# Kernel optimization log

Measured on AMD Instinct MI355X. Metric: run time of the kernel, lower is better.

## Reference

```python
import jax, jax.numpy as jnp
import numpy as np

B, T, D, H, WIN = 4, 2048, 512, 8, 128
DK = D // H
DFF = 4 * D
LN_EPS = 1e-5


def setup_inputs() -> dict:
    key = jax.random.key(0)
    ks = jax.random.split(key, 12)
    p = lambda k, shp: jax.random.normal(k, shp, jnp.float32) * 0.02
    return {
        "x": jax.random.normal(ks[0], (B, T, D), jnp.float32),
        "pad_mask": jnp.ones((B, T), dtype=bool),
        "wq": p(ks[1], (D, D)), "bq": jnp.zeros((D,), jnp.float32),
        "wk": p(ks[2], (D, D)), "bk": jnp.zeros((D,), jnp.float32),
        "wv": p(ks[3], (D, D)), "bv": jnp.zeros((D,), jnp.float32),
        "wo": p(ks[4], (D, D)), "bo": jnp.zeros((D,), jnp.float32),
        "w1": p(ks[5], (D, DFF)), "b1": jnp.zeros((DFF,), jnp.float32),
        "w2": p(ks[6], (DFF, D)), "b2": jnp.zeros((D,), jnp.float32),
        "g1": jnp.ones((D,), jnp.float32), "be1": jnp.zeros((D,), jnp.float32),
        "g2": jnp.ones((D,), jnp.float32), "be2": jnp.zeros((D,), jnp.float32),
    }


def _ln(x, g, b):
    m = x.mean(-1, keepdims=True)
    v = ((x - m) ** 2).mean(-1, keepdims=True)
    return (x - m) * jax.lax.rsqrt(v + LN_EPS) * g + b


def reference(x, pad_mask, wq, bq, wk, bk, wv, bv, wo, bo,
              w1, b1, w2, b2, g1, be1, g2, be2):
    Bv, Tv, Dv = x.shape
    # projections -> [B, H, T, DK]
    q = (x @ wq + bq).reshape(Bv, Tv, H, DK).transpose(0, 2, 1, 3)
    k = (x @ wk + bk).reshape(Bv, Tv, H, DK).transpose(0, 2, 1, 3)
    v = (x @ wv + bv).reshape(Bv, Tv, H, DK).transpose(0, 2, 1, 3)
    idx = jnp.arange(Tv)
    dist = idx[None, :] - idx[:, None]  # q rows, k cols? matches torch: idx[None,:]-idx[:,None] with rows=q
    wmask = (dist >= 0) & (dist < WIN)  # note: dist = k - q in torch code orientation; see original
    # original: dist = idx[None,:] - idx[:,None]; window_mask[q, k] = (k - q >= 0)&(k - q < W)? No:
    # torch uses dist[q, k] = idx[None,:][q,k] - idx[:,None][q,k] = k - q, mask (dist>=0)&(dist<W)
    # so key index >= query index within window — reproduce exactly.
    mask = pad_mask[:, None, None, :] & wmask[None, None, :, :]  # [B,1,T,T]
    scores = jnp.einsum('bhqd,bhkd->bhqk', q, k) / np.float32(np.sqrt(DK))
    scores = jnp.where(mask, scores, jnp.float32(-1e9))
    attn = jax.nn.softmax(scores, axis=-1)
    o = jnp.einsum('bhqk,bhkd->bhqd', attn, v)
    o = o.transpose(0, 2, 1, 3).reshape(Bv, Tv, Dv)
    attn_out = o @ wo + bo
    x1 = _ln(x + attn_out, g1, be1)
    ff = jax.nn.relu(x1 @ w1 + b1) @ w2 + b2
    return _ln(x1 + ff, g2, be2)
```

## Files before the change

### kernel.cpp

```cpp
#include <hip/hip_runtime.h>

typedef __bf16 bf16;
typedef float  f32x4  __attribute__((ext_vector_type(4)));
typedef __bf16 bf16x8 __attribute__((ext_vector_type(8)));
typedef __bf16 bf16x4 __attribute__((ext_vector_type(4)));

#define GLOAD_LDS16(gsrc, ldst) \
  __builtin_amdgcn_global_load_lds((const __attribute__((address_space(1))) void*)(gsrc), \
                                   (__attribute__((address_space(3))) void*)(ldst), 16, 0, 0)

constexpr int Bc   = 4;
constexpr int Tc   = 2048;
constexpr int Dc   = 512;
constexpr int Hc   = 8;
constexpr int DKc  = 64;
constexpr int DFFc = 2048;
constexpr int WINc = 128;
constexpr int Mr   = Bc * Tc;
constexpr size_t MD = (size_t)Mr * Dc;
constexpr int TVc  = 2176;

__device__ bf16  g_xb[MD];
__device__ bf16  g_wqkvT[3 * Dc * Dc];
__device__ bf16  g_woT[Dc * Dc];
__device__ bf16  g_w1T[DFFc * Dc];
__device__ bf16  g_w2T[Dc * DFFc];
__device__ float g_biasqkv[3 * Dc];
__device__ bf16  g_qkv[Mr * 3 * Dc];
__device__ bf16  g_vT[(size_t)Bc * Hc * DKc * TVc];
__device__ bf16  g_o[MD];
__device__ bf16  g_attnp[2 * MD];
__device__ bf16  g_x1b[MD];
__device__ bf16  g_ff1[Mr * DFFc];
__device__ bf16  g_ff2p[4 * MD];

__global__ __launch_bounds__(256) void prep_k(const float* __restrict__ x,
                                              const float* __restrict__ wq, const float* __restrict__ wk,
                                              const float* __restrict__ wv, const float* __restrict__ wo,
                                              const float* __restrict__ w1, const float* __restrict__ w2,
                                              const float* __restrict__ bq, const float* __restrict__ bk,
                                              const float* __restrict__ bv) {
  int bid = blockIdx.x;
  if (bid < 2048) {
    size_t i = (size_t)bid * 2048 + threadIdx.x * 8;
    float4 a = *(const float4*)(x + i);
    float4 c = *(const float4*)(x + i + 4);
    bf16x8 o;
    o[0] = (bf16)a.x; o[1] = (bf16)a.y; o[2] = (bf16)a.z; o[3] = (bf16)a.w;
    o[4] = (bf16)c.x; o[5] = (bf16)c.y; o[6] = (bf16)c.z; o[7] = (bf16)c.w;
    *(bf16x8*)(g_xb + i) = o;
    return;
  }
  if (bid >= 5120) {
    int i = (bid - 5120) * 256 + threadIdx.x;
    if (i < 1536) g_biasqkv[i] = (i < 512) ? bq[i] : (i < 1024 ? bk[i - 512] : bv[i - 1024]);
    return;
  }
  const float* W; bf16* dst; int K, N, nx, ky;
  if (bid < 3072) {
    int local = bid - 2048;
    int wsel = local >> 8; local &= 255;
    nx = local & 15; ky = local >> 4; K = 512; N = 512;
    switch (wsel) {
      case 0: W = wq; dst = g_wqkvT;              break;
      case 1: W = wk; dst = g_wqkvT + 512 * 512;  break;
      case 2: W = wv; dst = g_wqkvT + 1024 * 512; break;
      default:W = wo; dst = g_woT;                break;
    }
  } else if (bid < 4096) {
    int local = bid - 3072;
    nx = local & 63; ky = local >> 6; K = 512; N = 2048; W = w1; dst = g_w1T;
  } else {
    int local = bid - 4096;
    nx = local & 15; ky = local >> 4; K = 2048; N = 512; W = w2; dst = g_w2T;
  }
  __shared__ float t[32][33];
  int n0 = nx * 32, k0 = ky * 32;
  int tx = threadIdx.x & 31, ty = threadIdx.x >> 5;
  #pragma unroll
  for (int i = 0; i < 4; ++i)
    t[ty + i * 8][tx] = W[(size_t)(k0 + ty + i * 8) * N + n0 + tx];
  __syncthreads();
  #pragma unroll
  for (int i = 0; i < 4; ++i)
    dst[(size_t)(n0 + ty + i * 8) * K + k0 + tx] = (bf16)t[tx][ty + i * 8];
}

__global__ __launch_bounds__(512, 2) void gemm8p_k(int which, const float* __restrict__ bias_in) {
  const bf16 *A, *BT; bf16* Cb; const float* bias;
  int N, K; bool relu = false;
  int kz = blockIdx.z;
  if (which == 0)      { A = g_xb;  BT = g_wqkvT; Cb = g_qkv; bias = g_biasqkv; N = 1536; K = 512; }
  else if (which == 2) { A = g_x1b; BT = g_w1T;   Cb = g_ff1; bias = bias_in;   N = 2048; K = 512; relu = true; }
  else                 { A = g_ff1; BT = g_w2T;   Cb = g_ff2p + (size_t)kz * MD; bias = bias_in; N = 512; K = 2048; }
  if (kz) bias = nullptr;
  const int kzoff = kz * 512;
  constexpr int NT = 8;

  __shared__ __align__(16) bf16 lds[65536];

  const int tid = threadIdx.x;
  const int bm = blockIdx.x, bn = blockIdx.y;
  const int w = tid >> 6, lane = tid & 63;
  const int wm = w >> 2, wn = w & 3;
  const int r = lane & 15, gg = lane >> 4;

  const bf16* gA0 = A  + (size_t)(bm * 256) * K + kzoff;
  const bf16* gB0 = BT + (size_t)(bn * 256) * K + kzoff;

  f32x4 acc[8][4] = {};

  auto stageHalf = [&](int S) {
    if (S >= 4 * NT) return;
    const int tau = S >> 2, h = S & 3, buf = tau & 1;
    const int colT = tau * 64;
    if (h >= 2) {
      const int ks = h - 2;
      char* dst = (char*)lds + buf * 65536 + ks * 16384 + w * 1024;
      #pragma unroll
      for (int swp = 0; swp < 2; ++swp) {
        int s = swp * 512 + tid;
        int row = s >> 2;
        int cb = (s & 3) ^ (((row >> 1) ^ (row >> 3)) & 3);
        GLOAD_LDS16(gA0 + (size_t)row * K + colT + ks * 32 + cb * 8, dst + swp * 8192);
      }
    } else {
      char* dst = (char*)lds + buf * 65536 + 32768 + h * 16384 + w * 1024;
      #pragma unroll
      for (int swp = 0; swp < 2; ++swp) {
        int s = swp * 512 + tid;
        int row = h * 128 + (s >> 3);
        int cb = (s & 7) ^ (row & 7);
        GLOAD_LDS16(gB0 + (size_t)row * K + colT + cb * 8, dst + swp * 8192);
      }
    }
  };

  #pragma unroll
  for (int S = 0; S < 7; ++S) stageHalf(S);
  asm volatile("s_waitcnt vmcnt(6)" ::: "memory");
  __builtin_amdgcn_s_barrier();

  #pragma unroll
  for (int t = 0; t < NT; ++t) {
    const bf16* lb = lds + (t & 1) * 32768;
    bf16x8 b0[4], b1[4], afr[4];

    #pragma unroll
    for (int ni = 0; ni < 4; ++ni) {
      int row = wn * 64 + ni * 16 + r;
      b0[ni] = *(const bf16x8*)(lb + 16384 + row * 64 + ((gg ^ (r & 7)) << 3));
      b1[ni] = *(const bf16x8*)(lb + 16384 + row * 64 + (((4 + gg) ^ (r & 7)) << 3));
    }
    #pragma unroll
    for (int i = 0; i < 4; ++i) {
      int row = wm * 128 + i * 16 + r;
      afr[i] = *(const bf16x8*)(lb + row * 32 + ((gg ^ (((row >> 1) ^ (row >> 3)) & 3)) << 3));
    }
    asm volatile("" ::: "memory");
    stageHalf(4 * t + 7);
    __builtin_amdgcn_s_barrier();
    __builtin_amdgcn_s_setprio(1);
    #pragma unroll
    for (int i = 0; i < 4; ++i)
      #pragma unroll
      for (int ni = 0; ni < 4; ++ni)
        acc[i][ni] = __builtin_amdgcn_mfma_f32_16x16x32_bf16(afr[i], b0[ni], acc[i][ni], 0, 0, 0);
    __builtin_amdgcn_s_setprio(0);
    __builtin_amdgcn_s_barrier();

    #pragma unroll
    for (int i = 0; i < 4; ++i) {
      int row = wm * 128 + 64 + i * 16 + r;
      afr[i] = *(const bf16x8*)(lb + row * 32 + ((gg ^ (((row >> 1) ^ (row >> 3)) & 3)) << 3));
    }
    asm volatile("" ::: "memory");
    stageHalf(4 * t + 8);
    __builtin_amdgcn_s_barrier();
    __builtin_amdgcn_s_setprio(1);
    #pragma unroll
    for (int i = 0; i < 4; ++i)
      #pragma unroll
      for (int ni = 0; ni < 4; ++ni)
        acc[4 + i][ni] = __builtin_amdgcn_mfma_f32_16x16x32_bf16(afr[i], b0[ni], acc[4 + i][ni], 0, 0, 0);
    __builtin_amdgcn_s_setprio(0);
    __builtin_amdgcn_s_barrier();

    #pragma unroll
    for (int i = 0; i < 4; ++i) {
      int row = wm * 128 + i * 16 + r;
      afr[i] = *(const bf16x8*)(lb + 8192 + row * 32 + ((gg ^ (((row >> 1) ^ (row >> 3)) & 3)) << 3));
    }
    asm volatile("" ::: "memory");
    stageHalf(4 * t + 9);
    __builtin_amdgcn_s_barrier();
    __builtin_amdgcn_s_setprio(1);
    #pragma unroll
    for (int i = 0; i < 4; ++i)
      #pragma unroll
      for (int ni = 0; ni < 4; ++ni)
        acc[i][ni] = __builtin_amdgcn_mfma_f32_16x16x32_bf16(afr[i], b1[ni], acc[i][ni], 0, 0, 0);
    __builtin_amdgcn_s_setprio(0);
    __builtin_amdgcn_s_barrier();

    #pragma unroll
    for (int i = 0; i < 4; ++i) {
      int row = wm * 128 + 64 + i * 16 + r;
      afr[i] = *(const bf16x8*)(lb + 8192 + row * 32 + ((gg ^ (((row >> 1) ^ (row >> 3)) & 3)) << 3));
    }
    asm volatile("" ::: "memory");
    stageHalf(4 * t + 10);
    if (t < NT - 2)       asm volatile("s_waitcnt vmcnt(6)" ::: "memory");
    else if (t == NT - 2) asm volatile("s_waitcnt vmcnt(0)" ::: "memory");
    __builtin_amdgcn_s_barrier();
    __builtin_amdgcn_s_setprio(1);
    #pragma unroll
    for (int i = 0; i < 4; ++i)
      #pragma unroll
      for (int ni = 0; ni < 4; ++ni)
        acc[4 + i][ni] = __builtin_amdgcn_mfma_f32_16x16x32_bf16(afr[i], b1[ni], acc[4 + i][ni], 0, 0, 0);
    __builtin_amdgcn_s_setprio(0);
    __builtin_amdgcn_s_barrier();
  }

  if (which == 0 && bn >= 4) {
    #pragma unroll
    for (int mi = 0; mi < 8; ++mi) {
      int row0 = bm * 256 + wm * 128 + mi * 16 + gg * 4;
      int bidx = row0 >> 11, t0 = row0 & 2047;
      #pragma unroll
      for (int ni = 0; ni < 4; ++ni) {
        int col = bn * 256 + wn * 64 + ni * 16 + r;
        float bv = bias[col];
        int vcol = col - 1024;
        bf16x4 ov;
        #pragma unroll
        for (int j = 0; j < 4; ++j) ov[j] = (bf16)(acc[mi][ni][j] + bv);
        *(bf16x4*)(g_vT + (size_t)(bidx * 512 + vcol) * TVc + t0) = ov;
      }
    }
    return;
  }
  #pragma unroll
  for (int mi = 0; mi < 8; ++mi) {
    int row0 = bm * 256 + wm * 128 + mi * 16 + gg * 4;
    #pragma unroll
    for (int ni = 0; ni < 4; ++ni) {
      int col = bn * 256 + wn * 64 + ni * 16 + r;
      float bv = bias ? bias[col] : 0.f;
      #pragma unroll
      for (int j = 0; j < 4; ++j) {
        float v0 = acc[mi][ni][j] + bv;
        if (relu) v0 = fmaxf(v0, 0.f);
        Cb[(size_t)(row0 + j) * N + col] = (bf16)v0;
      }
    }
  }
}

__global__ __launch_bounds__(256) void gemm_k(const float* __restrict__ bias_in) {
  const bf16 *A, *BT;
  bf16* Cb;
  const float* bias;
  int N, K, Klen;
  int kz = blockIdx.z;
  { A = g_o; BT = g_woT; Cb = g_attnp + (size_t)kz * MD; bias = bias_in; N = 512; K = 512; Klen = 256; }
  if (kz) bias = nullptr;

  __shared__ __align__(16) bf16 lA[128 * 32];
  __shared__ __align__(16) bf16 lB[128 * 32];
  int tid = threadIdx.x;
  int bm = blockIdx.x, bn = blockIdx.y;
  int w = tid >> 6, lane = tid & 63;
  int wm = w >> 1, wn = w & 1;
  int r = lane & 15, gg = lane >> 4;

  f32x4 acc[4][4] = {};

  const bf16* gA = A + (size_t)(bm * 128 + (tid >> 2)) * K + (size_t)kz * Klen + (tid & 3) * 8;
  const bf16* gB = BT + (size_t)(bn * 128 + (tid >> 2)) * K + (size_t)kz * Klen + (tid & 3) * 8;
  char* lAb = (char*)lA + (tid & 0xC0) * 16;
  char* lBb = (char*)lB + (tid & 0xC0) * 16;

  for (int k0 = 0; k0 < Klen; k0 += 32) {
    GLOAD_LDS16(gA + k0,                  lAb);
    GLOAD_LDS16(gA + (size_t)64 * K + k0, lAb + 4096);
    GLOAD_LDS16(gB + k0,                  lBb);
    GLOAD_LDS16(gB + (size_t)64 * K + k0, lBb + 4096);
    asm volatile("s_waitcnt vmcnt(0)" ::: "memory");
    __syncthreads();
    bf16x8 afrag[4], bfrag[4];
    #pragma unroll
    for (int i = 0; i < 4; ++i)
      afrag[i] = *(const bf16x8*)(&lA[(wm * 64 + i * 16 + r) * 32 + gg * 8]);
    #pragma unroll
    for (int i = 0; i < 4; ++i)
      bfrag[i] = *(const bf16x8*)(&lB[(wn * 64 + i * 16 + r) * 32 + gg * 8]);
    #pragma unroll
    for (int mi = 0; mi < 4; ++mi)
      #pragma unroll
      for (int ni = 0; ni < 4; ++ni)
        acc[mi][ni] = __builtin_amdgcn_mfma_f32_16x16x32_bf16(afrag[mi], bfrag[ni], acc[mi][ni], 0, 0, 0);
    __syncthreads();
  }

  #pragma unroll
  for (int mi = 0; mi < 4; ++mi) {
    int row0 = bm * 128 + wm * 64 + mi * 16 + gg * 4;
    #pragma unroll
    for (int ni = 0; ni < 4; ++ni) {
      int col = bn * 128 + wn * 64 + ni * 16 + r;
      float bv = bias ? bias[col] : 0.f;
      #pragma unroll
      for (int j = 0; j < 4; ++j) {
        float v0 = acc[mi][ni][j] + bv;
        Cb[(size_t)(row0 + j) * N + col] = (bf16)v0;
      }
    }
  }
}

__global__ __launch_bounds__(256) void attn_k() {
  constexpr int KT = 192;
  __shared__ __align__(16) bf16 lKP[KT * 64];
  __shared__ __align__(16) bf16 lVT[64 * KT];
  int tid = threadIdx.x;
  int qt = blockIdx.x, bh = blockIdx.y;
  int b = bh >> 3, h = bh & 7;
  int q0 = qt * 64;
  int w = tid >> 6, lane = tid & 63;
  int r = lane & 15, gg = lane >> 4;

  {
    const bf16* kbase = g_qkv + (size_t)b * Tc * 1536 + 512 + h * 64;
    char* ldst = (char*)lKP + w * 1024;
    #pragma unroll
    for (int p = 0; p < 6; ++p) {
      int s = p * 256 + tid;
      int key = s >> 3;
      int cb = (s & 7) ^ (key & 7);
      int gkey = q0 + key;
      int srow = gkey < Tc ? gkey : 0;
      GLOAD_LDS16(kbase + (size_t)srow * 1536 + cb * 8, ldst + p * 4096);
    }
  }
  {
    const bf16* vbase = g_vT + (size_t)(bh * 64) * TVc + q0;
    char* ldst = (char*)lVT + w * 1024;
    #pragma unroll
    for (int p = 0; p < 6; ++p) {
      int s = p * 256 + tid;
      int d = s / 24;
      int sc = s - d * 24;
      int cb = sc ^ (d & 7);
      GLOAD_LDS16(vbase + (size_t)d * TVc + cb * 8, ldst + p * 4096);
    }
  }
  bf16x8 qf0, qf1;
  {
    int qrow = q0 + w * 16 + r;
    const bf16* qp = g_qkv + (size_t)(b * Tc + qrow) * 1536 + h * 64;
    qf0 = *(const bf16x8*)(qp + gg * 8);
    qf1 = *(const bf16x8*)(qp + 32 + gg * 8);
  }
  asm volatile("s_waitcnt vmcnt(0)" ::: "memory");
  __syncthreads();

  f32x4 s[12] = {};
  #pragma unroll
  for (int ni = 0; ni < 12; ++ni) {
    int key = ni * 16 + r;
    int sw = key & 7;
    bf16x8 k0f = *(const bf16x8*)(&lKP[key * 64 + ((gg ^ sw) << 3)]);
    bf16x8 k1f = *(const bf16x8*)(&lKP[key * 64 + (((4 | gg) ^ sw) << 3)]);
    s[ni] = __builtin_amdgcn_mfma_f32_16x16x32_bf16(qf0, k0f, s[ni], 0, 0, 0);
    s[ni] = __builtin_amdgcn_mfma_f32_16x16x32_bf16(qf1, k1f, s[ni], 0, 0, 0);
  }

  float mx[4] = {-3e38f, -3e38f, -3e38f, -3e38f};
  #pragma unroll
  for (int ni = 0; ni < 12; ++ni)
    #pragma unroll
    for (int j = 0; j < 4; ++j) {
      int qloc = w * 16 + gg * 4 + j;
      int col = ni * 16 + r;
      bool valid = (col >= qloc) && (col < qloc + WINc) && (q0 + col < Tc);
      float sv = valid ? s[ni][j] * 0.125f : -3e38f;
      s[ni][j] = sv;
      mx[j] = fmaxf(mx[j], sv);
    }
  #pragma unroll
  for (int m = 1; m < 16; m <<= 1)
    #pragma unroll
    for (int j = 0; j < 4; ++j) mx[j] = fmaxf(mx[j], __shfl_xor(mx[j], m, 64));

  float sm[4] = {0.f, 0.f, 0.f, 0.f};
  #pragma unroll
  for (int ni = 0; ni < 12; ++ni)
    #pragma unroll
    for (int j = 0; j < 4; ++j) {
      float p = __expf(s[ni][j] - mx[j]);
      s[ni][j] = p;
      sm[j] += p;
    }
  #pragma unroll
  for (int m = 1; m < 16; m <<= 1)
    #pragma unroll
    for (int j = 0; j < 4; ++j) sm[j] += __shfl_xor(sm[j], m, 64);

  __syncthreads();
  #pragma unroll
  for (int ni = 0; ni < 12; ++ni)
    #pragma unroll
    for (int j = 0; j < 4; ++j) {
      int q = w * 16 + gg * 4 + j;
      int col = ni * 16 + r;
      int idx = q * KT + ((((col >> 3) ^ (q & 7)) << 3) | (col & 7));
      lKP[idx] = (bf16)s[ni][j];
    }
  __syncthreads();

  f32x4 o[4] = {};
  int swl = r & 7;
  #pragma unroll
  for (int ks = 0; ks < 6; ++ks) {
    int ch = ((ks * 4 + gg) ^ swl) << 3;
    bf16x8 pf = *(const bf16x8*)(&lKP[(w * 16 + r) * KT + ch]);
    #pragma unroll
    for (int nf = 0; nf < 4; ++nf) {
      bf16x8 vf = *(const bf16x8*)(&lVT[(nf * 16 + r) * KT + ch]);
      o[nf] = __builtin_amdgcn_mfma_f32_16x16x32_bf16(pf, vf, o[nf], 0, 0, 0);
    }
  }
  #pragma unroll
  for (int nf = 0; nf < 4; ++nf) {
    int dk = nf * 16 + r;
    #pragma unroll
    for (int j = 0; j < 4; ++j) {
      int qloc = w * 16 + gg * 4 + j;
      float ov = o[nf][j] / sm[j];
      g_o[(size_t)(b * Tc + q0 + qloc) * Dc + h * 64 + dk] = (bf16)ov;
    }
  }
}

__global__ __launch_bounds__(256) void ln_k(int which, const float* __restrict__ gw,
                                            const float* __restrict__ bw,
                                            float* __restrict__ outf_in) {
  int row = blockIdx.x * 4 + (threadIdx.x >> 6);
  int lane = threadIdx.x & 63;
  const bf16* a; const bf16* pb; int np; float* outf; bf16* outb;
  if (which == 0) { a = g_xb;  pb = g_attnp; np = 2; outf = nullptr;  outb = g_x1b; }
  else            { a = g_x1b; pb = g_ff2p;  np = 4; outf = outf_in;  outb = nullptr; }
  size_t off = (size_t)row * 512 + lane * 8;
  bf16x8 av = *(const bf16x8*)(a + off);
  float v[8];
  #pragma unroll
  for (int i = 0; i < 8; ++i) v[i] = (float)av[i];
  for (int p = 0; p < np; ++p) {
    bf16x8 t = *(const bf16x8*)(pb + (size_t)p * MD + off);
    #pragma unroll
    for (int i = 0; i < 8; ++i) v[i] += (float)t[i];
  }
  float s = 0.f;
  #pragma unroll
  for (int i = 0; i < 8; ++i) s += v[i];
  #pragma unroll
  for (int m = 1; m < 64; m <<= 1) s += __shfl_xor(s, m, 64);
  float mean = s * (1.0f / 512.0f);
  float q = 0.f;
  #pragma unroll
  for (int i = 0; i < 8; ++i) { float d = v[i] - mean; q += d * d; }
  #pragma unroll
  for (int m = 1; m < 64; m <<= 1) q += __shfl_xor(q, m, 64);
  float rstd = rsqrtf(q * (1.0f / 512.0f) + 1e-5f);
  float4 g0 = *(const float4*)(gw + lane * 8), g1v = *(const float4*)(gw + lane * 8 + 4);
  float4 e0 = *(const float4*)(bw + lane * 8), e1 = *(const float4*)(bw + lane * 8 + 4);
  float gg[8] = {g0.x, g0.y, g0.z, g0.w, g1v.x, g1v.y, g1v.z, g1v.w};
  float bb[8] = {e0.x, e0.y, e0.z, e0.w, e1.x, e1.y, e1.z, e1.w};
  float o[8];
  #pragma unroll
  for (int i = 0; i < 8; ++i) o[i] = (v[i] - mean) * rstd * gg[i] + bb[i];
  if (outf) {
    float4 o0 = {o[0], o[1], o[2], o[3]}, o1 = {o[4], o[5], o[6], o[7]};
    *(float4*)(outf + off) = o0;
    *(float4*)(outf + off + 4) = o1;
  }
  if (outb) {
    bf16x8 ob;
    #pragma unroll
    for (int i = 0; i < 8; ++i) ob[i] = (bf16)o[i];
    *(bf16x8*)(outb + off) = ob;
  }
}

extern "C" void kernel_launch(void* const* d_in, const int* in_sizes, int n_in,
                              void* d_out, int out_size, void* d_ws, size_t ws_size,
                              hipStream_t stream) {
  const float* x   = (const float*)d_in[0];
  const float* wq  = (const float*)d_in[2];
  const float* bq  = (const float*)d_in[3];
  const float* wk  = (const float*)d_in[4];
  const float* bk  = (const float*)d_in[5];
  const float* wv  = (const float*)d_in[6];
  const float* bv  = (const float*)d_in[7];
  const float* wo  = (const float*)d_in[8];
  const float* bo  = (const float*)d_in[9];
  const float* w1  = (const float*)d_in[10];
  const float* b1  = (const float*)d_in[11];
  const float* w2  = (const float*)d_in[12];
  const float* b2  = (const float*)d_in[13];
  const float* g1  = (const float*)d_in[14];
  const float* be1 = (const float*)d_in[15];
  const float* g2  = (const float*)d_in[16];
  const float* be2 = (const float*)d_in[17];
  float* out = (float*)d_out;

  prep_k<<<5126, 256, 0, stream>>>(x, wq, wk, wv, wo, w1, w2, bq, bk, bv);

  gemm8p_k<<<dim3(32, 6, 1), 512, 0, stream>>>(0, nullptr);
  attn_k<<<dim3(32, 32), 256, 0, stream>>>();
  gemm_k<<<dim3(64, 4, 2), 256, 0, stream>>>(bo);
  ln_k<<<2048, 256, 0, stream>>>(0, g1, be1, nullptr);
  gemm8p_k<<<dim3(32, 8, 1), 512, 0, stream>>>(2, b1);
  gemm8p_k<<<dim3(32, 2, 4), 512, 0, stream>>>(3, b2);
  ln_k<<<2048, 256, 0, stream>>>(1, g2, be2, out);
}
```

Measured before the change: 145.1 us.

## Remap block indices for XCD-aware L2 locality and overlap V loads in attention

Remaps the linear block id in the three GEMM/attention kernels so that consecutive blocks, which the hardware spreads round-robin across the XCDs, share A/B tiles or neighbouring query tiles on the same XCD's L2. In attention, the Q fragment loads are moved ahead of the V-tile loads, and the first barrier waits only for K (vmcnt(6)), so the QK^T and softmax work overlaps with the V transfer. The remapping assumes specific grid dimensions (32 or 64 in x), and the partial waitcnt depends on the exact count and order of outstanding loads.

```diff
diff --git a/kernel.cpp b/kernel.cpp
--- a/kernel.cpp
+++ b/kernel.cpp
@@ -87,20 +87,25 @@
 }
 
 __global__ __launch_bounds__(512, 2) void gemm8p_k(int which, const float* __restrict__ bias_in) {
+  const int h = blockIdx.x + 32 * (blockIdx.y + gridDim.y * blockIdx.z);
+  const int xc = h & 7, hi = h >> 3;
+  const int bm = xc + 8 * (hi & 3);
+  const int yz = hi >> 2;
+  const int bn = yz % gridDim.y;
+  const int kz = yz / gridDim.y;
+
   const bf16 *A, *BT; bf16* Cb; const float* bias;
   int N, K; bool relu = false;
-  int kz = blockIdx.z;
   if (which == 0)      { A = g_xb;  BT = g_wqkvT; Cb = g_qkv; bias = g_biasqkv; N = 1536; K = 512; }
   else if (which == 2) { A = g_x1b; BT = g_w1T;   Cb = g_ff1; bias = bias_in;   N = 2048; K = 512; relu = true; }
   else                 { A = g_ff1; BT = g_w2T;   Cb = g_ff2p + (size_t)kz * MD; bias = bias_in; N = 512; K = 2048; }
-  if (kz) bias = nullptr;
+  const float* bias0 = (kz == 0) ? bias : nullptr;
   const int kzoff = kz * 512;
   constexpr int NT = 8;
 
   __shared__ __align__(16) bf16 lds[65536];
 
   const int tid = threadIdx.x;
-  const int bm = blockIdx.x, bn = blockIdx.y;
   const int w = tid >> 6, lane = tid & 63;
   const int wm = w >> 2, wn = w & 3;
   const int r = lane & 15, gg = lane >> 4;
@@ -112,10 +117,10 @@
 
   auto stageHalf = [&](int S) {
     if (S >= 4 * NT) return;
-    const int tau = S >> 2, h = S & 3, buf = tau & 1;
+    const int tau = S >> 2, hh = S & 3, buf = tau & 1;
     const int colT = tau * 64;
-    if (h >= 2) {
-      const int ks = h - 2;
+    if (hh >= 2) {
+      const int ks = hh - 2;
       char* dst = (char*)lds + buf * 65536 + ks * 16384 + w * 1024;
       #pragma unroll
       for (int swp = 0; swp < 2; ++swp) {
@@ -125,11 +130,11 @@
         GLOAD_LDS16(gA0 + (size_t)row * K + colT + ks * 32 + cb * 8, dst + swp * 8192);
       }
     } else {
-      char* dst = (char*)lds + buf * 65536 + 32768 + h * 16384 + w * 1024;
+      char* dst = (char*)lds + buf * 65536 + 32768 + hh * 16384 + w * 1024;
       #pragma unroll
       for (int swp = 0; swp < 2; ++swp) {
         int s = swp * 512 + tid;
-        int row = h * 128 + (s >> 3);
+        int row = hh * 128 + (s >> 3);
         int cb = (s & 7) ^ (row & 7);
         GLOAD_LDS16(gB0 + (size_t)row * K + colT + cb * 8, dst + swp * 8192);
       }
@@ -247,7 +252,7 @@
     #pragma unroll
     for (int ni = 0; ni < 4; ++ni) {
       int col = bn * 256 + wn * 64 + ni * 16 + r;
-      float bv = bias ? bias[col] : 0.f;
+      float bv = bias0 ? bias0[col] : 0.f;
       #pragma unroll
       for (int j = 0; j < 4; ++j) {
         float v0 = acc[mi][ni][j] + bv;
@@ -259,18 +264,20 @@
 }
 
 __global__ __launch_bounds__(256) void gemm_k(const float* __restrict__ bias_in) {
-  const bf16 *A, *BT;
-  bf16* Cb;
-  const float* bias;
-  int N, K, Klen;
-  int kz = blockIdx.z;
-  { A = g_o; BT = g_woT; Cb = g_attnp + (size_t)kz * MD; bias = bias_in; N = 512; K = 512; Klen = 256; }
-  if (kz) bias = nullptr;
+  const int h = blockIdx.x + 64 * (blockIdx.y + 4 * blockIdx.z);
+  const int xc = h & 7, hi = h >> 3;
+  const int bm = xc + 8 * (hi & 7);
+  const int yz = hi >> 3;
+  const int bn = yz & 3, kz = yz >> 2;
+
+  const bf16* A = g_o; const bf16* BT = g_woT;
+  bf16* Cb = g_attnp + (size_t)kz * MD;
+  const float* bias = kz ? nullptr : bias_in;
+  const int N = 512, K = 512, Klen = 256;
 
   __shared__ __align__(16) bf16 lA[128 * 32];
   __shared__ __align__(16) bf16 lB[128 * 32];
   int tid = threadIdx.x;
-  int bm = blockIdx.x, bn = blockIdx.y;
   int w = tid >> 6, lane = tid & 63;
   int wm = w >> 1, wn = w & 1;
   int r = lane & 15, gg = lane >> 4;
@@ -325,14 +332,17 @@
   __shared__ __align__(16) bf16 lKP[KT * 64];
   __shared__ __align__(16) bf16 lVT[64 * KT];
   int tid = threadIdx.x;
-  int qt = blockIdx.x, bh = blockIdx.y;
-  int b = bh >> 3, h = bh & 7;
+  const int h = blockIdx.x + 32 * blockIdx.y;
+  const int xc = h & 7, hi = h >> 3;
+  const int qt = 4 * xc + (hi & 3);
+  const int bh = hi >> 2;
+  int b = bh >> 3, hd = bh & 7;
   int q0 = qt * 64;
   int w = tid >> 6, lane = tid & 63;
   int r = lane & 15, gg = lane >> 4;
 
   {
-    const bf16* kbase = g_qkv + (size_t)b * Tc * 1536 + 512 + h * 64;
+    const bf16* kbase = g_qkv + (size_t)b * Tc * 1536 + 512 + hd * 64;
     char* ldst = (char*)lKP + w * 1024;
     #pragma unroll
     for (int p = 0; p < 6; ++p) {
@@ -344,6 +354,15 @@
       GLOAD_LDS16(kbase + (size_t)srow * 1536 + cb * 8, ldst + p * 4096);
     }
   }
+  __builtin_amdgcn_sched_barrier(0);
+  bf16x8 qf0, qf1;
+  {
+    int qrow = q0 + w * 16 + r;
+    const bf16* qp = g_qkv + (size_t)(b * Tc + qrow) * 1536 + hd * 64;
+    qf0 = *(const bf16x8*)(qp + gg * 8);
+    qf1 = *(const bf16x8*)(qp + 32 + gg * 8);
+  }
+  __builtin_amdgcn_sched_barrier(0);
   {
     const bf16* vbase = g_vT + (size_t)(bh * 64) * TVc + q0;
     char* ldst = (char*)lVT + w * 1024;
@@ -356,15 +375,8 @@
       GLOAD_LDS16(vbase + (size_t)d * TVc + cb * 8, ldst + p * 4096);
     }
   }
-  bf16x8 qf0, qf1;
-  {
-    int qrow = q0 + w * 16 + r;
-    const bf16* qp = g_qkv + (size_t)(b * Tc + qrow) * 1536 + h * 64;
-    qf0 = *(const bf16x8*)(qp + gg * 8);
-    qf1 = *(const bf16x8*)(qp + 32 + gg * 8);
-  }
-  asm volatile("s_waitcnt vmcnt(0)" ::: "memory");
-  __syncthreads();
+  asm volatile("s_waitcnt vmcnt(6)" ::: "memory");
+  __builtin_amdgcn_s_barrier();
 
   f32x4 s[12] = {};
   #pragma unroll
@@ -408,7 +420,7 @@
     #pragma unroll
     for (int j = 0; j < 4; ++j) sm[j] += __shfl_xor(sm[j], m, 64);
 
-  __syncthreads();
+  __builtin_amdgcn_s_barrier();
   #pragma unroll
   for (int ni = 0; ni < 12; ++ni)
     #pragma unroll
@@ -418,7 +430,8 @@
       int idx = q * KT + ((((col >> 3) ^ (q & 7)) << 3) | (col & 7));
       lKP[idx] = (bf16)s[ni][j];
     }
-  __syncthreads();
+  asm volatile("s_waitcnt vmcnt(0) lgkmcnt(0)" ::: "memory");
+  __builtin_amdgcn_s_barrier();
 
   f32x4 o[4] = {};
   int swl = r & 7;
@@ -439,7 +452,7 @@
     for (int j = 0; j < 4; ++j) {
       int qloc = w * 16 + gg * 4 + j;
       float ov = o[nf][j] / sm[j];
-      g_o[(size_t)(b * Tc + q0 + qloc) * Dc + h * 64 + dk] = (bf16)ov;
+      g_o[(size_t)(b * Tc + q0 + qloc) * Dc + hd * 64 + dk] = (bf16)ov;
     }
   }
 }
```

Result: no change. 144.1 us (-0.7%).
